# Optimization experiments

Measured on AMD Instinct MI355X. Metric: run time of the kernel, lower is better.

The kernel has to match this reference:

```python
import jax, jax.numpy as jnp
import numpy as np

B, N, L, D, H = 2, 2048, 2048, 1024, 16
HD = D // H  # 64


def setup_inputs() -> dict:
    key = jax.random.key(0)
    ks = jax.random.split(key, 12)
    s = 0.02
    return {
        "x_q": jax.random.normal(ks[0], (B, N, D), jnp.float32),
        "x_kv": jax.random.normal(ks[1], (B, L, D), jnp.float32),
        "pad_mask": jax.random.randint(ks[2], (B, L), 0, 2) > 0,
        "wq": jax.random.normal(ks[3], (D, D), jnp.float32) * s,
        "bq": jnp.zeros((D,), jnp.float32),
        "wk": jax.random.normal(ks[4], (D, D), jnp.float32) * s,
        "bk": jnp.zeros((D,), jnp.float32),
        "wv": jax.random.normal(ks[5], (D, D), jnp.float32) * s,
        "bv": jnp.zeros((D,), jnp.float32),
        "wo": jax.random.normal(ks[6], (D, D), jnp.float32) * s,
        "bo": jnp.zeros((D,), jnp.float32),
    }


def reference(x_q, x_kv, pad_mask, wq, bq, wk, bk, wv, bv, wo, bo):
    scale = HD ** -0.5
    # projections: (B, S, D) -> (B, H, S, HD)
    def split_heads(x):
        return x.reshape(x.shape[0], x.shape[1], H, HD).transpose(0, 2, 1, 3)
    q = split_heads(x_q @ wq + bq) * scale
    k = split_heads(x_kv @ wk + bk)
    v = split_heads(x_kv @ wv + bv)
    attn = jnp.einsum('bhic,bhjc->bhij', q, k)  # (B, H, N, L)
    neg = -jnp.finfo(attn.dtype).max
    attn = jnp.where(pad_mask[:, None, None, :], neg, attn)
    attn = jax.nn.softmax(attn, axis=-1)
    o = jnp.einsum('bhij,bhjc->bhic', attn, v)  # (B, H, N, HD)
    o = o.transpose(0, 2, 1, 3).reshape(B, N, D)
    return o @ wo + bo
```

## Files before the change

kernel.cpp:

```cpp
#include <hip/hip_runtime.h>
#include <hip/hip_bf16.h>
#include <math.h>

typedef __bf16 bf16;
typedef __attribute__((ext_vector_type(8))) __bf16 bf16x8;
typedef __attribute__((ext_vector_type(4))) __bf16 bf16x4;
typedef __attribute__((ext_vector_type(4))) float floatx4;
typedef __attribute__((ext_vector_type(16))) float floatx16;

#define BB 2
#define NN 2048
#define LL 2048
#define DD 1024
#define HH 16
#define HDD 64

#define QSCALE (0.125f * 1.44269504f)
#define PCLAMP 21.66f
#define MBIAS  (-100000.0f)

__device__ __forceinline__ void async16(const bf16* g, bf16* l) {
  __builtin_amdgcn_global_load_lds((const __attribute__((address_space(1))) void*)(g),
                                   (__attribute__((address_space(3))) void*)(l), 16, 0, 0);
}

__global__ __launch_bounds__(256) void prep_kernel(
    const float* __restrict__ xq, const float* __restrict__ xkv,
    bf16* __restrict__ Xqb, bf16* __restrict__ Xkvb, int nconv, int elemsEach,
    const float* __restrict__ W0, const float* __restrict__ W1,
    const float* __restrict__ W2, const float* __restrict__ W3,
    bf16* __restrict__ T0, bf16* __restrict__ T1,
    bf16* __restrict__ T2, bf16* __restrict__ T3,
    const unsigned* __restrict__ mask, float* __restrict__ biasF)
{
  __shared__ bf16 Tb[64][72];
  const int bid = blockIdx.x;
  const int t = threadIdx.x;

  if (bid < nconv) {
    const int half = nconv >> 1;
    const float* s = (bid < half) ? xq : xkv;
    bf16* d = (bid < half) ? Xqb : Xkvb;
    int gid = (bid < half) ? bid : bid - half;
    int idx = (gid * 256 + t) * 8;
    if (idx >= elemsEach) return;
    floatx4 a = *(const floatx4*)&s[idx];
    floatx4 b = *(const floatx4*)&s[idx + 4];
    bf16x8 o;
#pragma unroll
    for (int e = 0; e < 4; e++) { o[e] = (bf16)a[e]; o[4 + e] = (bf16)b[e]; }
    *(bf16x8*)&d[idx] = o;
    return;
  }
  if (bid < nconv + 1024) {
    const int wb = bid - nconv;
    const int which = wb >> 8;
    const float* W = which == 0 ? W0 : which == 1 ? W1 : which == 2 ? W2 : W3;
    bf16*       T = which == 0 ? T0 : which == 1 ? T1 : which == 2 ? T2 : T3;
    const int tile = wb & 255;
    const int k0 = (tile >> 4) * 64, n0 = (tile & 15) * 64;
    const int r = t >> 2;
    const int c = (t & 3) * 16;
    const float* Wr = W + (size_t)(k0 + r) * 1024 + n0 + c;
    floatx4 f0 = *(const floatx4*)(Wr + 0);
    floatx4 f1 = *(const floatx4*)(Wr + 4);
    floatx4 f2 = *(const floatx4*)(Wr + 8);
    floatx4 f3 = *(const floatx4*)(Wr + 12);
#pragma unroll
    for (int e = 0; e < 4; e++) {
      Tb[c + e][r]      = (bf16)f0[e];
      Tb[c + 4 + e][r]  = (bf16)f1[e];
      Tb[c + 8 + e][r]  = (bf16)f2[e];
      Tb[c + 12 + e][r] = (bf16)f3[e];
    }
    __syncthreads();
    bf16* Tr = T + (size_t)(n0 + r) * 1024 + k0 + c;
    *(bf16x8*)&Tr[0] = *(const bf16x8*)&Tb[r][c];
    *(bf16x8*)&Tr[8] = *(const bf16x8*)&Tb[r][c + 8];
    return;
  }
  __shared__ int hasBig, hasFloat;
  if (t == 0) { hasBig = 0; hasFloat = 0; }
  __syncthreads();
  int big = 0, flt = 0;
  for (int idx = t; idx < 1024; idx += 256) {
    unsigned v = mask[idx];
    if (v == 0x3F800000u) flt = 1;
    else if (v > 1u) big = 1;
  }
  if (big) atomicOr(&hasBig, 1);
  if (flt) atomicOr(&hasFloat, 1);
  __syncthreads();
  const int mode = hasFloat ? 2 : (hasBig ? 1 : 0);
  for (int k = t * 16; k < t * 16 + 16; k++) {
    bool m;
    if (mode == 0)      m = ((const int*)mask)[k] != 0;
    else if (mode == 1) m = ((const unsigned char*)mask)[k] != 0;
    else                m = ((const float*)mask)[k] != 0.0f;
    biasF[k] = m ? MBIAS : 0.0f;
  }
}

template <typename TC>
__device__ __forceinline__ void gemm_body32(
    int bx, const bf16* __restrict__ A, const bf16* __restrict__ Wt,
    const float* __restrict__ bias, TC* __restrict__ C, float scale, int transv)
{
  __shared__ bf16 As[128 * 64];
  __shared__ bf16 Bs[128 * 64];

  const int tm = bx >> 3, tn = bx & 7;
  const int m0 = tm * 128, n0 = tn * 128;
  const int t = threadIdx.x;
  const int w = t >> 6, l = t & 63;
  const int col = l & 31, half = l >> 5;
  const int wm = (w >> 1) * 64, wn = (w & 1) * 64;
  const int sr  = t >> 3;
  const int scl = (t & 7) * 8;
  const int scs = (((t & 7) ^ (sr & 7)) * 8);
  const int csw = col & 7;

  floatx16 acc[2][2];
#pragma unroll
  for (int mi = 0; mi < 2; mi++)
#pragma unroll
    for (int ni = 0; ni < 2; ni++)
#pragma unroll
      for (int e = 0; e < 16; e++) acc[mi][ni][e] = 0.0f;

  for (int k0 = 0; k0 < 1024; k0 += 64) {
    __syncthreads();
#pragma unroll
    for (int j = 0; j < 4; j++)
      async16(&A[(size_t)(m0 + j * 32 + sr) * 1024 + k0 + scs], &As[(j * 32 + sr) * 64 + scl]);
#pragma unroll
    for (int j = 0; j < 4; j++)
      async16(&Wt[(size_t)(n0 + j * 32 + sr) * 1024 + k0 + scs], &Bs[(j * 32 + sr) * 64 + scl]);
    __syncthreads();
#pragma unroll
    for (int kk = 0; kk < 4; kk++) {
      const int ch = ((kk * 2 + half) ^ csw) * 8;
      bf16x8 af[2], bfr[2];
#pragma unroll
      for (int mi = 0; mi < 2; mi++)
        af[mi] = *(const bf16x8*)&As[(wm + mi * 32 + col) * 64 + ch];
#pragma unroll
      for (int ni = 0; ni < 2; ni++)
        bfr[ni] = *(const bf16x8*)&Bs[(wn + ni * 32 + col) * 64 + ch];
#pragma unroll
      for (int mi = 0; mi < 2; mi++)
#pragma unroll
        for (int ni = 0; ni < 2; ni++)
          acc[mi][ni] = __builtin_amdgcn_mfma_f32_32x32x16_bf16(af[mi], bfr[ni], acc[mi][ni], 0, 0, 0);
    }
  }
#pragma unroll
  for (int ni = 0; ni < 2; ni++) {
    int colg = n0 + wn + ni * 32 + col;
    float bv = bias[colg];
#pragma unroll
    for (int mi = 0; mi < 2; mi++) {
      int rbase = m0 + wm + mi * 32 + half * 4;
      if (transv) {
#pragma unroll
        for (int g = 0; g < 4; g++) {
          int key0 = rbase + g * 8;
          int bb = key0 >> 11, key = key0 & 2047;
          bf16x4 v4;
#pragma unroll
          for (int r = 0; r < 4; r++) v4[r] = (bf16)(acc[mi][ni][g * 4 + r] + bv);
          *(bf16x4*)&((bf16*)C)[(size_t)bb * (DD * (size_t)LL) + (size_t)colg * LL + key] = v4;
        }
      } else {
#pragma unroll
        for (int g = 0; g < 4; g++)
#pragma unroll
          for (int r = 0; r < 4; r++)
            C[(size_t)(rbase + g * 8 + r) * 1024 + colg] = (TC)((acc[mi][ni][g * 4 + r] + bv) * scale);
      }
    }
  }
}

__global__ __launch_bounds__(256) void qkv_gemm32(
    const bf16* __restrict__ Xq, const bf16* __restrict__ Xkv,
    const bf16* __restrict__ Wtq, const bf16* __restrict__ Wtk, const bf16* __restrict__ Wtv,
    const float* __restrict__ bq, const float* __restrict__ bk, const float* __restrict__ bv,
    bf16* __restrict__ Qp, bf16* __restrict__ Kp, bf16* __restrict__ VtG, int shift)
{
  const int bid = blockIdx.x;
  const int which = bid >> shift;
  const int bx = bid & ((1 << shift) - 1);
  if (which == 0)      gemm_body32<bf16>(bx, Xq,  Wtq, bq, Qp,  QSCALE, 0);
  else if (which == 1) gemm_body32<bf16>(bx, Xkv, Wtk, bk, Kp,  1.0f,   0);
  else                 gemm_body32<bf16>(bx, Xkv, Wtv, bv, VtG, 1.0f,   1);
}

__global__ __launch_bounds__(256) void out_gemm(
    const bf16* __restrict__ A, const bf16* __restrict__ Wt,
    const float* __restrict__ bias, float* __restrict__ C)
{
  __shared__ bf16 As[128 * 64];
  __shared__ bf16 Bs[64 * 64];

  const int bx = blockIdx.x;
  const int tm = bx >> 4, tn = bx & 15;
  const int m0 = tm * 128, n0 = tn * 64;
  const int t = threadIdx.x;
  const int w = t >> 6, l = t & 63;
  const int q = l >> 4, i = l & 15;
  const int wm = (w >> 1) * 64, wn = (w & 1) * 32;
  const int sr  = t >> 3;
  const int scl = (t & 7) * 8;
  const int scs = (((t & 7) ^ (sr & 7)) * 8);
  const int isw = i & 7;

  const floatx4 zero = {0.f, 0.f, 0.f, 0.f};
  floatx4 acc[4][2];
#pragma unroll
  for (int mi = 0; mi < 4; mi++)
#pragma unroll
    for (int ni = 0; ni < 2; ni++) acc[mi][ni] = zero;

  for (int k0 = 0; k0 < 1024; k0 += 64) {
    __syncthreads();
#pragma unroll
    for (int j = 0; j < 4; j++)
      async16(&A[(size_t)(m0 + j * 32 + sr) * 1024 + k0 + scs], &As[(j * 32 + sr) * 64 + scl]);
#pragma unroll
    for (int j = 0; j < 2; j++)
      async16(&Wt[(size_t)(n0 + j * 32 + sr) * 1024 + k0 + scs], &Bs[(j * 32 + sr) * 64 + scl]);
    __syncthreads();
#pragma unroll
    for (int ks = 0; ks < 2; ks++) {
#pragma unroll
      for (int qq = 0; qq < 1; qq++) {}
      const int ch = ((ks * 4 + q) ^ isw) * 8;
      bf16x8 af[4], bfr[2];
#pragma unroll
      for (int mi = 0; mi < 4; mi++)
        af[mi] = *(const bf16x8*)&As[(wm + mi * 16 + i) * 64 + ch];
#pragma unroll
      for (int ni = 0; ni < 2; ni++)
        bfr[ni] = *(const bf16x8*)&Bs[(wn + ni * 16 + i) * 64 + ch];
#pragma unroll
      for (int mi = 0; mi < 4; mi++)
#pragma unroll
        for (int ni = 0; ni < 2; ni++)
          acc[mi][ni] = __builtin_amdgcn_mfma_f32_16x16x32_bf16(af[mi], bfr[ni], acc[mi][ni], 0, 0, 0);
    }
  }
#pragma unroll
  for (int ni = 0; ni < 2; ni++) {
    int colg = n0 + wn + ni * 16 + i;
    float bv = bias[colg];
#pragma unroll
    for (int mi = 0; mi < 4; mi++) {
      int row = m0 + wm + mi * 16 + q * 4;
#pragma unroll
      for (int r = 0; r < 4; r++)
        C[(size_t)(row + r) * 1024 + colg] = acc[mi][ni][r] + bv;
    }
  }
}

__global__ __launch_bounds__(256) void attn_kernel(
    const bf16* __restrict__ Q, const bf16* __restrict__ K,
    const bf16* __restrict__ Vt, const float* __restrict__ biasF,
    bf16* __restrict__ O, int hbits)
{
  __shared__ bf16 Ks[64][72];
  __shared__ bf16 Vs[64][72];
  __shared__ bf16 Ps[4][16][72];

  const int bid = blockIdx.x;
  const int qt = bid >> hbits;
  const int hb = bid & ((1 << hbits) - 1);
  const int h  = (hbits == 5) ? (hb >> 1) : hb;
  const int b  = (hbits == 5) ? (hb & 1) : 0;
  const int t = threadIdx.x;
  const int w = t >> 6, lane = t & 63;
  const int q = lane >> 4, i = lane & 15;

  const bf16* Qb = Q  + (size_t)b * (NN * DD) + h * HDD;
  const bf16* Kb = K  + (size_t)b * (LL * DD) + h * HDD;
  const bf16* Vb = Vt + (size_t)b * (DD * (size_t)LL) + (size_t)(h * HDD) * LL;
  const float* biasFb = biasF + b * LL;

  const int qrow = qt * 64 + w * 16;
  bf16x8 qfrag[2];
#pragma unroll
  for (int ks = 0; ks < 2; ks++)
    qfrag[ks] = *(const bf16x8*)&Qb[(size_t)(qrow + i) * DD + ks * 32 + q * 8];

  floatx4 oacc[4];
#pragma unroll
  for (int n = 0; n < 4; n++) {
#pragma unroll
    for (int r = 0; r < 4; r++) oacc[n][r] = 0.0f;
  }
  float psum = 0.0f;

  const int ldr = t >> 3;
  const int ldc = (t & 7) * 8;

  bf16x8 pk0 = *(const bf16x8*)&Kb[(size_t)ldr * DD + ldc];
  bf16x8 pk1 = *(const bf16x8*)&Kb[(size_t)(ldr + 32) * DD + ldc];
  bf16x8 pv0 = *(const bf16x8*)&Vb[(size_t)ldr * LL + ldc];
  bf16x8 pv1 = *(const bf16x8*)&Vb[(size_t)(ldr + 32) * LL + ldc];
  floatx4 pb[4];
#pragma unroll
  for (int n = 0; n < 4; n++)
    pb[n] = *(const floatx4*)&biasFb[n * 16 + q * 4];

  for (int kt = 0; kt < LL; kt += 64) {
    __syncthreads();
    *(bf16x8*)&Ks[ldr][ldc]      = pk0;
    *(bf16x8*)&Ks[ldr + 32][ldc] = pk1;
    *(bf16x8*)&Vs[ldr][ldc]      = pv0;
    *(bf16x8*)&Vs[ldr + 32][ldc] = pv1;
    __syncthreads();

    {
      const int ktn = (kt + 64) & (LL - 1);
      pk0 = *(const bf16x8*)&Kb[(size_t)(ktn + ldr) * DD + ldc];
      pk1 = *(const bf16x8*)&Kb[(size_t)(ktn + ldr + 32) * DD + ldc];
      pv0 = *(const bf16x8*)&Vb[(size_t)ldr * LL + ktn + ldc];
      pv1 = *(const bf16x8*)&Vb[(size_t)(ldr + 32) * LL + ktn + ldc];
    }

#pragma unroll
    for (int n = 0; n < 4; n++) {
      floatx4 a = pb[n];
#pragma unroll
      for (int ks = 0; ks < 2; ks++) {
        bf16x8 kf = *(const bf16x8*)&Ks[n * 16 + i][ks * 32 + q * 8];
        a = __builtin_amdgcn_mfma_f32_16x16x32_bf16(kf, qfrag[ks], a, 0, 0, 0);
      }
      bf16x4 v4;
#pragma unroll
      for (int r = 0; r < 4; r++) {
        float p = __builtin_amdgcn_exp2f(fminf(a[r], PCLAMP));
        psum += p;
        v4[r] = (bf16)p;
      }
      *(bf16x4*)&Ps[w][i][n * 16 + q * 4] = v4;
    }
    {
      const int ktn = (kt + 64) & (LL - 1);
#pragma unroll
      for (int n = 0; n < 4; n++)
        pb[n] = *(const floatx4*)&biasFb[ktn + n * 16 + q * 4];
    }
    bf16x8 pf[2];
#pragma unroll
    for (int ks = 0; ks < 2; ks++)
      pf[ks] = *(const bf16x8*)&Ps[w][i][ks * 32 + q * 8];
#pragma unroll
    for (int n = 0; n < 4; n++) {
#pragma unroll
      for (int ks = 0; ks < 2; ks++) {
        bf16x8 vf = *(const bf16x8*)&Vs[n * 16 + i][ks * 32 + q * 8];
        oacc[n] = __builtin_amdgcn_mfma_f32_16x16x32_bf16(vf, pf[ks], oacc[n], 0, 0, 0);
      }
    }
  }

  psum += __shfl_xor(psum, 16, 64);
  psum += __shfl_xor(psum, 32, 64);
  float inv = 1.0f / fmaxf(psum, 1e-30f);

  bf16* Ob = O + (size_t)b * (NN * DD) + h * HDD;
#pragma unroll
  for (int n = 0; n < 4; n++) {
    bf16x4 v4;
#pragma unroll
    for (int r = 0; r < 4; r++) v4[r] = (bf16)(oacc[n][r] * inv);
    *(bf16x4*)&Ob[(size_t)(qrow + i) * DD + n * 16 + q * 4] = v4;
  }
}

extern "C" void kernel_launch(void* const* d_in, const int* in_sizes, int n_in,
                              void* d_out, int out_size, void* d_ws, size_t ws_size,
                              hipStream_t stream)
{
  const float* x_q  = (const float*)d_in[0];
  const float* x_kv = (const float*)d_in[1];
  const void*  pad  = d_in[2];
  const float* wq = (const float*)d_in[3];
  const float* bq = (const float*)d_in[4];
  const float* wk = (const float*)d_in[5];
  const float* bk = (const float*)d_in[6];
  const float* wv = (const float*)d_in[7];
  const float* bv = (const float*)d_in[8];
  const float* wo = (const float*)d_in[9];
  const float* bo = (const float*)d_in[10];
  float* out = (float*)d_out;

  char* ws = (char*)d_ws;
  const size_t MB = (size_t)1 << 20;
  const size_t fullElems = (size_t)BB * NN * DD;
  const size_t batchElems = (size_t)NN * DD;

  if (ws_size >= 49 * MB) {
    bf16* Xqb   = (bf16*)(ws);
    bf16* Xkvb  = (bf16*)(ws + 8 * MB);
    bf16* Wtq   = (bf16*)(ws + 16 * MB);
    bf16* Wtk   = (bf16*)(ws + 18 * MB);
    bf16* Wtv   = (bf16*)(ws + 20 * MB);
    bf16* Wto   = (bf16*)(ws + 22 * MB);
    bf16* Qp    = (bf16*)(ws + 24 * MB);
    bf16* Kp    = (bf16*)(ws + 32 * MB);
    bf16* VtG   = (bf16*)(ws + 40 * MB);
    float* biasF = (float*)(ws + 48 * MB);
    bf16* Op    = Xqb;

    prep_kernel<<<5121, 256, 0, stream>>>(x_q, x_kv, Xqb, Xkvb, 4096, (int)fullElems,
                                          wq, wk, wv, wo, Wtq, Wtk, Wtv, Wto,
                                          (const unsigned*)pad, biasF);
    qkv_gemm32<<<768, 256, 0, stream>>>(Xqb, Xkvb, Wtq, Wtk, Wtv, bq, bk, bv, Qp, Kp, VtG, 8);
    attn_kernel<<<1024, 256, 0, stream>>>(Qp, Kp, VtG, biasF, Op, 5);
    out_gemm<<<512, 256, 0, stream>>>(Op, Wto, bo, out);
  } else {
    bf16* Wtq   = (bf16*)(ws);
    bf16* Wtk   = (bf16*)(ws + 2 * MB);
    bf16* Wtv   = (bf16*)(ws + 4 * MB);
    bf16* Wto   = (bf16*)(ws + 6 * MB);
    bf16* Xqb   = (bf16*)(ws + 8 * MB);
    bf16* Xkvb  = (bf16*)(ws + 12 * MB);
    bf16* Qp    = (bf16*)(ws + 16 * MB);
    bf16* Kp    = (bf16*)(ws + 20 * MB);
    bf16* VtG   = (bf16*)(ws + 24 * MB);
    float* biasF = (float*)(ws + 28 * MB);
    bf16* Op    = Xqb;

    for (int b = 0; b < BB; b++) {
      if (b == 0)
        prep_kernel<<<3073, 256, 0, stream>>>(x_q, x_kv, Xqb, Xkvb, 2048, (int)batchElems,
                                              wq, wk, wv, wo, Wtq, Wtk, Wtv, Wto,
                                              (const unsigned*)pad, biasF);
      else
        prep_kernel<<<2048, 256, 0, stream>>>(x_q + b * batchElems, x_kv + b * batchElems,
                                              Xqb, Xkvb, 2048, (int)batchElems,
                                              wq, wk, wv, wo, Wtq, Wtk, Wtv, Wto,
                                              (const unsigned*)pad, biasF);
      qkv_gemm32<<<384, 256, 0, stream>>>(Xqb, Xkvb, Wtq, Wtk, Wtv, bq, bk, bv, Qp, Kp, VtG, 7);
      attn_kernel<<<512, 256, 0, stream>>>(Qp, Kp, VtG, biasF + b * LL, Op, 4);
      out_gemm<<<256, 256, 0, stream>>>(Op, Wto, bo, out + b * batchElems);
    }
  }
}
```

Measured before the change: 242.0 us.

## Process two 16-row query tiles per wave in attention kernel

Each wave now handles 32 query rows instead of 16, so every block covers 128 queries and the grid is halved. K and V fragments read from shared memory are reused across both query sub-tiles, and each block's K/V global loads serve twice as many queries. The trade-off is more registers (accumulators, Q fragments, P fragments) and a larger P buffer in shared memory. That can lower occupancy, and halving the grid to 512 blocks cuts the parallelism available across the CUs.

```diff
diff --git a/kernel.cpp b/kernel.cpp
--- a/kernel.cpp
+++ b/kernel.cpp
@@ -233,8 +233,6 @@
     __syncthreads();
 #pragma unroll
     for (int ks = 0; ks < 2; ks++) {
-#pragma unroll
-      for (int qq = 0; qq < 1; qq++) {}
       const int ch = ((ks * 4 + q) ^ isw) * 8;
       bf16x8 af[4], bfr[2];
 #pragma unroll
@@ -271,7 +269,7 @@
 {
   __shared__ bf16 Ks[64][72];
   __shared__ bf16 Vs[64][72];
-  __shared__ bf16 Ps[4][16][72];
+  __shared__ bf16 Ps[4][32][72];
 
   const int bid = blockIdx.x;
   const int qt = bid >> hbits;
@@ -287,19 +285,23 @@
   const bf16* Vb = Vt + (size_t)b * (DD * (size_t)LL) + (size_t)(h * HDD) * LL;
   const float* biasFb = biasF + b * LL;
 
-  const int qrow = qt * 64 + w * 16;
-  bf16x8 qfrag[2];
-#pragma unroll
-  for (int ks = 0; ks < 2; ks++)
-    qfrag[ks] = *(const bf16x8*)&Qb[(size_t)(qrow + i) * DD + ks * 32 + q * 8];
-
-  floatx4 oacc[4];
-#pragma unroll
-  for (int n = 0; n < 4; n++) {
-#pragma unroll
-    for (int r = 0; r < 4; r++) oacc[n][r] = 0.0f;
-  }
-  float psum = 0.0f;
+  const int qrow = qt * 128 + w * 32;
+  bf16x8 qfrag[2][2];
+#pragma unroll
+  for (int qq = 0; qq < 2; qq++)
+#pragma unroll
+    for (int ks = 0; ks < 2; ks++)
+      qfrag[qq][ks] = *(const bf16x8*)&Qb[(size_t)(qrow + qq * 16 + i) * DD + ks * 32 + q * 8];
+
+  floatx4 oacc[2][4];
+#pragma unroll
+  for (int qq = 0; qq < 2; qq++)
+#pragma unroll
+    for (int n = 0; n < 4; n++) {
+#pragma unroll
+      for (int r = 0; r < 4; r++) oacc[qq][n][r] = 0.0f;
+    }
+  float psum[2] = {0.0f, 0.0f};
 
   const int ldr = t >> 3;
   const int ldc = (t & 7) * 8;
@@ -331,20 +333,22 @@
 
 #pragma unroll
     for (int n = 0; n < 4; n++) {
-      floatx4 a = pb[n];
-#pragma unroll
-      for (int ks = 0; ks < 2; ks++) {
-        bf16x8 kf = *(const bf16x8*)&Ks[n * 16 + i][ks * 32 + q * 8];
-        a = __builtin_amdgcn_mfma_f32_16x16x32_bf16(kf, qfrag[ks], a, 0, 0, 0);
+      bf16x8 kf0 = *(const bf16x8*)&Ks[n * 16 + i][q * 8];
+      bf16x8 kf1 = *(const bf16x8*)&Ks[n * 16 + i][32 + q * 8];
+#pragma unroll
+      for (int qq = 0; qq < 2; qq++) {
+        floatx4 a = pb[n];
+        a = __builtin_amdgcn_mfma_f32_16x16x32_bf16(kf0, qfrag[qq][0], a, 0, 0, 0);
+        a = __builtin_amdgcn_mfma_f32_16x16x32_bf16(kf1, qfrag[qq][1], a, 0, 0, 0);
+        bf16x4 v4;
+#pragma unroll
+        for (int r = 0; r < 4; r++) {
+          float p = __builtin_amdgcn_exp2f(fminf(a[r], PCLAMP));
+          psum[qq] += p;
+          v4[r] = (bf16)p;
+        }
+        *(bf16x4*)&Ps[w][qq * 16 + i][n * 16 + q * 4] = v4;
       }
-      bf16x4 v4;
-#pragma unroll
-      for (int r = 0; r < 4; r++) {
-        float p = __builtin_amdgcn_exp2f(fminf(a[r], PCLAMP));
-        psum += p;
-        v4[r] = (bf16)p;
-      }
-      *(bf16x4*)&Ps[w][i][n * 16 + q * 4] = v4;
     }
     {
       const int ktn = (kt + 64) & (LL - 1);
@@ -352,31 +356,38 @@
       for (int n = 0; n < 4; n++)
         pb[n] = *(const floatx4*)&biasFb[ktn + n * 16 + q * 4];
     }
-    bf16x8 pf[2];
-#pragma unroll
-    for (int ks = 0; ks < 2; ks++)
-      pf[ks] = *(const bf16x8*)&Ps[w][i][ks * 32 + q * 8];
+    bf16x8 pf[2][2];
+#pragma unroll
+    for (int qq = 0; qq < 2; qq++)
+#pragma unroll
+      for (int ks = 0; ks < 2; ks++)
+        pf[qq][ks] = *(const bf16x8*)&Ps[w][qq * 16 + i][ks * 32 + q * 8];
 #pragma unroll
     for (int n = 0; n < 4; n++) {
-#pragma unroll
-      for (int ks = 0; ks < 2; ks++) {
-        bf16x8 vf = *(const bf16x8*)&Vs[n * 16 + i][ks * 32 + q * 8];
-        oacc[n] = __builtin_amdgcn_mfma_f32_16x16x32_bf16(vf, pf[ks], oacc[n], 0, 0, 0);
+      bf16x8 vf0 = *(const bf16x8*)&Vs[n * 16 + i][q * 8];
+      bf16x8 vf1 = *(const bf16x8*)&Vs[n * 16 + i][32 + q * 8];
+#pragma unroll
+      for (int qq = 0; qq < 2; qq++) {
+        oacc[qq][n] = __builtin_amdgcn_mfma_f32_16x16x32_bf16(vf0, pf[qq][0], oacc[qq][n], 0, 0, 0);
+        oacc[qq][n] = __builtin_amdgcn_mfma_f32_16x16x32_bf16(vf1, pf[qq][1], oacc[qq][n], 0, 0, 0);
       }
     }
   }
 
-  psum += __shfl_xor(psum, 16, 64);
-  psum += __shfl_xor(psum, 32, 64);
-  float inv = 1.0f / fmaxf(psum, 1e-30f);
-
   bf16* Ob = O + (size_t)b * (NN * DD) + h * HDD;
 #pragma unroll
-  for (int n = 0; n < 4; n++) {
-    bf16x4 v4;
-#pragma unroll
-    for (int r = 0; r < 4; r++) v4[r] = (bf16)(oacc[n][r] * inv);
-    *(bf16x4*)&Ob[(size_t)(qrow + i) * DD + n * 16 + q * 4] = v4;
+  for (int qq = 0; qq < 2; qq++) {
+    float ps = psum[qq];
+    ps += __shfl_xor(ps, 16, 64);
+    ps += __shfl_xor(ps, 32, 64);
+    float inv = 1.0f / fmaxf(ps, 1e-30f);
+#pragma unroll
+    for (int n = 0; n < 4; n++) {
+      bf16x4 v4;
+#pragma unroll
+      for (int r = 0; r < 4; r++) v4[r] = (bf16)(oacc[qq][n][r] * inv);
+      *(bf16x4*)&Ob[(size_t)(qrow + qq * 16 + i) * DD + n * 16 + q * 4] = v4;
+    }
   }
 }
 
@@ -419,7 +430,7 @@
                                           wq, wk, wv, wo, Wtq, Wtk, Wtv, Wto,
                                           (const unsigned*)pad, biasF);
     qkv_gemm32<<<768, 256, 0, stream>>>(Xqb, Xkvb, Wtq, Wtk, Wtv, bq, bk, bv, Qp, Kp, VtG, 8);
-    attn_kernel<<<1024, 256, 0, stream>>>(Qp, Kp, VtG, biasF, Op, 5);
+    attn_kernel<<<512, 256, 0, stream>>>(Qp, Kp, VtG, biasF, Op, 5);
     out_gemm<<<512, 256, 0, stream>>>(Op, Wto, bo, out);
   } else {
     bf16* Wtq   = (bf16*)(ws);
@@ -445,7 +456,7 @@
                                               wq, wk, wv, wo, Wtq, Wtk, Wtv, Wto,
                                               (const unsigned*)pad, biasF);
       qkv_gemm32<<<384, 256, 0, stream>>>(Xqb, Xkvb, Wtq, Wtk, Wtv, bq, bk, bv, Qp, Kp, VtG, 7);
-      attn_kernel<<<512, 256, 0, stream>>>(Qp, Kp, VtG, biasF + b * LL, Op, 4);
+      attn_kernel<<<256, 256, 0, stream>>>(Qp, Kp, VtG, biasF + b * LL, Op, 4);
       out_gemm<<<256, 256, 0, stream>>>(Op, Wto, bo, out + b * batchElems);
     }
   }
```

New measurement: 235.1 us. -2.9%, faster.

## Rewrite attention with 32x32 MFMA, register P-fragments, and async double-buffered K/V

Applied to the files above, without the earlier changes.

The attention kernel moves from 16x16x32 to 32x32x16 bf16 MFMA, so each wave handles 32 query rows and each block 128 rows, which halves the grid. The probability tile is no longer staged through shared memory: packed bf16 conversions plus permlane32 swaps rebuild the B-operand fragment in registers. K/V tiles are loaded with global_load_lds into XOR-swizzled double buffers, so each iteration needs one barrier instead of two. The goal is less LDS traffic and less synchronization. The cost is more register pressure and only 512 blocks, which lowers occupancy.

```diff
diff --git a/kernel.cpp b/kernel.cpp
--- a/kernel.cpp
+++ b/kernel.cpp
@@ -22,6 +22,24 @@
 __device__ __forceinline__ void async16(const bf16* g, bf16* l) {
   __builtin_amdgcn_global_load_lds((const __attribute__((address_space(1))) void*)(g),
                                    (__attribute__((address_space(3))) void*)(l), 16, 0, 0);
+}
+
+__device__ __forceinline__ unsigned cvtpk(float a, float b) {
+  unsigned r;
+  asm("v_cvt_pk_bf16_f32 %0, %1, %2" : "=v"(r) : "v"(a), "v"(b));
+  return r;
+}
+
+__device__ __forceinline__ void plswap(unsigned &x, unsigned &y) {
+  auto r = __builtin_amdgcn_permlane32_swap(x, y, false, false);
+  x = (unsigned)r[0];
+  y = (unsigned)r[1];
+}
+
+__device__ __forceinline__ bf16x8 mk_frag(unsigned w0, unsigned w1, unsigned w2, unsigned w3) {
+  union { unsigned u[4]; bf16x8 b; } f;
+  f.u[0] = w0; f.u[1] = w1; f.u[2] = w2; f.u[3] = w3;
+  return f.b;
 }
 
 __global__ __launch_bounds__(256) void prep_kernel(
@@ -233,8 +251,6 @@
     __syncthreads();
 #pragma unroll
     for (int ks = 0; ks < 2; ks++) {
-#pragma unroll
-      for (int qq = 0; qq < 1; qq++) {}
       const int ch = ((ks * 4 + q) ^ isw) * 8;
       bf16x8 af[4], bfr[2];
 #pragma unroll
@@ -262,6 +278,71 @@
         C[(size_t)(row + r) * 1024 + colg] = acc[mi][ni][r] + bv;
     }
   }
+}
+
+__device__ __forceinline__ void attn_tile(
+    const bf16* __restrict__ Kg, const bf16* __restrict__ Vg,
+    const float* __restrict__ biasFb, int ktn,
+    const bf16* Kc, const bf16* Vc, bf16* Kn, bf16* Vn,
+    int sr, int scl, int scs, int col, int hi, int lsw,
+    const bf16x8* qfrag, floatx4 (*pb)[4], floatx16* oacc, float& psum)
+{
+  async16(&Kg[(size_t)(ktn + sr) * DD + scs],      Kn + sr * 64 + scl);
+  async16(&Kg[(size_t)(ktn + sr + 32) * DD + scs], Kn + (sr + 32) * 64 + scl);
+  async16(&Vg[(size_t)sr * LL + ktn + scs],        Vn + sr * 64 + scl);
+  async16(&Vg[(size_t)(sr + 32) * LL + ktn + scs], Vn + (sr + 32) * 64 + scl);
+
+  floatx16 sacc[2];
+#pragma unroll
+  for (int kb = 0; kb < 2; kb++)
+#pragma unroll
+    for (int g = 0; g < 4; g++)
+#pragma unroll
+      for (int rr = 0; rr < 4; rr++)
+        sacc[kb][g * 4 + rr] = pb[kb][g][rr];
+
+#pragma unroll
+  for (int kb = 0; kb < 2; kb++)
+#pragma unroll
+    for (int dc = 0; dc < 4; dc++) {
+      bf16x8 kf = *(const bf16x8*)&Kc[(kb * 32 + col) * 64 + ((dc * 2 + hi) ^ lsw) * 8];
+      sacc[kb] = __builtin_amdgcn_mfma_f32_32x32x16_bf16(kf, qfrag[dc], sacc[kb], 0, 0, 0);
+    }
+
+#pragma unroll
+  for (int kb = 0; kb < 2; kb++)
+#pragma unroll
+    for (int g = 0; g < 4; g++)
+      pb[kb][g] = *(const floatx4*)&biasFb[ktn + kb * 32 + g * 8 + hi * 4];
+
+  bf16x8 pfrag[4];
+#pragma unroll
+  for (int kb = 0; kb < 2; kb++)
+#pragma unroll
+    for (int hh = 0; hh < 2; hh++) {
+      float pv[8];
+#pragma unroll
+      for (int e = 0; e < 8; e++) {
+        float p = __builtin_amdgcn_exp2f(fminf(sacc[kb][hh * 8 + e], PCLAMP));
+        psum += p;
+        pv[e] = p;
+      }
+      unsigned a0 = cvtpk(pv[0], pv[1]);
+      unsigned a1 = cvtpk(pv[2], pv[3]);
+      unsigned b0 = cvtpk(pv[4], pv[5]);
+      unsigned b1 = cvtpk(pv[6], pv[7]);
+      plswap(a0, b0);
+      plswap(a1, b1);
+      pfrag[kb * 2 + hh] = mk_frag(a0, a1, b0, b1);
+    }
+
+#pragma unroll
+  for (int db = 0; db < 2; db++)
+#pragma unroll
+    for (int kc = 0; kc < 4; kc++) {
+      bf16x8 vf = *(const bf16x8*)&Vc[(db * 32 + col) * 64 + ((kc * 2 + hi) ^ lsw) * 8];
+      oacc[db] = __builtin_amdgcn_mfma_f32_32x32x16_bf16(vf, pfrag[kc], oacc[db], 0, 0, 0);
+    }
 }
 
 __global__ __launch_bounds__(256) void attn_kernel(
@@ -269,9 +350,8 @@
     const bf16* __restrict__ Vt, const float* __restrict__ biasF,
     bf16* __restrict__ O, int hbits)
 {
-  __shared__ bf16 Ks[64][72];
-  __shared__ bf16 Vs[64][72];
-  __shared__ bf16 Ps[4][16][72];
+  __shared__ bf16 Kbuf[2][64 * 64];
+  __shared__ bf16 Vbuf[2][64 * 64];
 
   const int bid = blockIdx.x;
   const int qt = bid >> hbits;
@@ -280,104 +360,72 @@
   const int b  = (hbits == 5) ? (hb & 1) : 0;
   const int t = threadIdx.x;
   const int w = t >> 6, lane = t & 63;
-  const int q = lane >> 4, i = lane & 15;
+  const int col = lane & 31;
+  const int hi  = lane >> 5;
+  const int lsw = lane & 7;
 
   const bf16* Qb = Q  + (size_t)b * (NN * DD) + h * HDD;
   const bf16* Kb = K  + (size_t)b * (LL * DD) + h * HDD;
   const bf16* Vb = Vt + (size_t)b * (DD * (size_t)LL) + (size_t)(h * HDD) * LL;
   const float* biasFb = biasF + b * LL;
 
-  const int qrow = qt * 64 + w * 16;
-  bf16x8 qfrag[2];
-#pragma unroll
-  for (int ks = 0; ks < 2; ks++)
-    qfrag[ks] = *(const bf16x8*)&Qb[(size_t)(qrow + i) * DD + ks * 32 + q * 8];
-
-  floatx4 oacc[4];
-#pragma unroll
-  for (int n = 0; n < 4; n++) {
-#pragma unroll
-    for (int r = 0; r < 4; r++) oacc[n][r] = 0.0f;
-  }
+  const int qrow = qt * 128 + w * 32;
+
+  bf16x8 qfrag[4];
+#pragma unroll
+  for (int dc = 0; dc < 4; dc++)
+    qfrag[dc] = *(const bf16x8*)&Qb[(size_t)(qrow + col) * DD + dc * 16 + hi * 8];
+
+  floatx16 oacc[2];
+#pragma unroll
+  for (int db = 0; db < 2; db++)
+#pragma unroll
+    for (int e = 0; e < 16; e++) oacc[db][e] = 0.0f;
   float psum = 0.0f;
 
-  const int ldr = t >> 3;
-  const int ldc = (t & 7) * 8;
-
-  bf16x8 pk0 = *(const bf16x8*)&Kb[(size_t)ldr * DD + ldc];
-  bf16x8 pk1 = *(const bf16x8*)&Kb[(size_t)(ldr + 32) * DD + ldc];
-  bf16x8 pv0 = *(const bf16x8*)&Vb[(size_t)ldr * LL + ldc];
-  bf16x8 pv1 = *(const bf16x8*)&Vb[(size_t)(ldr + 32) * LL + ldc];
-  floatx4 pb[4];
-#pragma unroll
-  for (int n = 0; n < 4; n++)
-    pb[n] = *(const floatx4*)&biasFb[n * 16 + q * 4];
+  const int sr  = t >> 3;
+  const int scl = (t & 7) * 8;
+  const int scs = ((t & 7) ^ (sr & 7)) * 8;
+
+  async16(&Kb[(size_t)sr * DD + scs],        &Kbuf[0][sr * 64 + scl]);
+  async16(&Kb[(size_t)(sr + 32) * DD + scs], &Kbuf[0][(sr + 32) * 64 + scl]);
+  async16(&Vb[(size_t)sr * LL + scs],        &Vbuf[0][sr * 64 + scl]);
+  async16(&Vb[(size_t)(sr + 32) * LL + scs], &Vbuf[0][(sr + 32) * 64 + scl]);
+
+  floatx4 pb[2][4];
+#pragma unroll
+  for (int kb = 0; kb < 2; kb++)
+#pragma unroll
+    for (int g = 0; g < 4; g++)
+      pb[kb][g] = *(const floatx4*)&biasFb[kb * 32 + g * 8 + hi * 4];
+
+  __syncthreads();
+
+  const bf16 *Kc = &Kbuf[0][0], *Vc = &Vbuf[0][0];
+  bf16 *Kn = &Kbuf[1][0], *Vn = &Vbuf[1][0];
 
   for (int kt = 0; kt < LL; kt += 64) {
+    const int ktn = (kt + 64) & (LL - 1);
+    attn_tile(Kb, Vb, biasFb, ktn, Kc, Vc, Kn, Vn,
+              sr, scl, scs, col, hi, lsw, qfrag, pb, oacc, psum);
+    const bf16* tk = Kc; Kc = Kn; Kn = (bf16*)tk;
+    const bf16* tv = Vc; Vc = Vn; Vn = (bf16*)tv;
     __syncthreads();
-    *(bf16x8*)&Ks[ldr][ldc]      = pk0;
-    *(bf16x8*)&Ks[ldr + 32][ldc] = pk1;
-    *(bf16x8*)&Vs[ldr][ldc]      = pv0;
-    *(bf16x8*)&Vs[ldr + 32][ldc] = pv1;
-    __syncthreads();
-
-    {
-      const int ktn = (kt + 64) & (LL - 1);
-      pk0 = *(const bf16x8*)&Kb[(size_t)(ktn + ldr) * DD + ldc];
-      pk1 = *(const bf16x8*)&Kb[(size_t)(ktn + ldr + 32) * DD + ldc];
-      pv0 = *(const bf16x8*)&Vb[(size_t)ldr * LL + ktn + ldc];
-      pv1 = *(const bf16x8*)&Vb[(size_t)(ldr + 32) * LL + ktn + ldc];
-    }
-
-#pragma unroll
-    for (int n = 0; n < 4; n++) {
-      floatx4 a = pb[n];
-#pragma unroll
-      for (int ks = 0; ks < 2; ks++) {
-        bf16x8 kf = *(const bf16x8*)&Ks[n * 16 + i][ks * 32 + q * 8];
-        a = __builtin_amdgcn_mfma_f32_16x16x32_bf16(kf, qfrag[ks], a, 0, 0, 0);
-      }
-      bf16x4 v4;
-#pragma unroll
-      for (int r = 0; r < 4; r++) {
-        float p = __builtin_amdgcn_exp2f(fminf(a[r], PCLAMP));
-        psum += p;
-        v4[r] = (bf16)p;
-      }
-      *(bf16x4*)&Ps[w][i][n * 16 + q * 4] = v4;
-    }
-    {
-      const int ktn = (kt + 64) & (LL - 1);
-#pragma unroll
-      for (int n = 0; n < 4; n++)
-        pb[n] = *(const floatx4*)&biasFb[ktn + n * 16 + q * 4];
-    }
-    bf16x8 pf[2];
-#pragma unroll
-    for (int ks = 0; ks < 2; ks++)
-      pf[ks] = *(const bf16x8*)&Ps[w][i][ks * 32 + q * 8];
-#pragma unroll
-    for (int n = 0; n < 4; n++) {
-#pragma unroll
-      for (int ks = 0; ks < 2; ks++) {
-        bf16x8 vf = *(const bf16x8*)&Vs[n * 16 + i][ks * 32 + q * 8];
-        oacc[n] = __builtin_amdgcn_mfma_f32_16x16x32_bf16(vf, pf[ks], oacc[n], 0, 0, 0);
-      }
-    }
-  }
-
-  psum += __shfl_xor(psum, 16, 64);
+  }
+
   psum += __shfl_xor(psum, 32, 64);
   float inv = 1.0f / fmaxf(psum, 1e-30f);
 
   bf16* Ob = O + (size_t)b * (NN * DD) + h * HDD;
 #pragma unroll
-  for (int n = 0; n < 4; n++) {
-    bf16x4 v4;
-#pragma unroll
-    for (int r = 0; r < 4; r++) v4[r] = (bf16)(oacc[n][r] * inv);
-    *(bf16x4*)&Ob[(size_t)(qrow + i) * DD + n * 16 + q * 4] = v4;
-  }
+  for (int db = 0; db < 2; db++)
+#pragma unroll
+    for (int g = 0; g < 4; g++) {
+      bf16x4 v4;
+#pragma unroll
+      for (int rr = 0; rr < 4; rr++) v4[rr] = (bf16)(oacc[db][g * 4 + rr] * inv);
+      *(bf16x4*)&Ob[(size_t)(qrow + col) * DD + db * 32 + g * 8 + hi * 4] = v4;
+    }
 }
 
 extern "C" void kernel_launch(void* const* d_in, const int* in_sizes, int n_in,
@@ -419,7 +467,7 @@
                                           wq, wk, wv, wo, Wtq, Wtk, Wtv, Wto,
                                           (const unsigned*)pad, biasF);
     qkv_gemm32<<<768, 256, 0, stream>>>(Xqb, Xkvb, Wtq, Wtk, Wtv, bq, bk, bv, Qp, Kp, VtG, 8);
-    attn_kernel<<<1024, 256, 0, stream>>>(Qp, Kp, VtG, biasF, Op, 5);
+    attn_kernel<<<512, 256, 0, stream>>>(Qp, Kp, VtG, biasF, Op, 5);
     out_gemm<<<512, 256, 0, stream>>>(Op, Wto, bo, out);
   } else {
     bf16* Wtq   = (bf16*)(ws);
@@ -445,7 +493,7 @@
                                               wq, wk, wv, wo, Wtq, Wtk, Wtv, Wto,
                                               (const unsigned*)pad, biasF);
       qkv_gemm32<<<384, 256, 0, stream>>>(Xqb, Xkvb, Wtq, Wtk, Wtv, bq, bk, bv, Qp, Kp, VtG, 7);
-      attn_kernel<<<512, 256, 0, stream>>>(Qp, Kp, VtG, biasF + b * LL, Op, 4);
+      attn_kernel<<<256, 256, 0, stream>>>(Qp, Kp, VtG, biasF + b * LL, Op, 4);
       out_gemm<<<256, 256, 0, stream>>>(Op, Wto, bo, out + b * batchElems);
     }
   }
```

Result: faster. 234.8 us (-3.0%).
